# Optimization experiments

Hardware: AMD Instinct MI355X
Metric: run time of the kernel (lower is better)

## Reference

```python
import jax, jax.numpy as jnp
import numpy as np

B, H, W, C = 4, 64, 64, 128  # input feature map; num_heads == filters == C


def setup_inputs() -> dict:
    key = jax.random.key(0)
    ks = jax.random.split(key, 5)
    x = jax.random.normal(ks[0], (B, H, W, C), dtype=jnp.float32)
    scale = 0.02  # keep QK^T logits in a sane range for softmax
    Wf = jax.random.normal(ks[1], (C, C), dtype=jnp.float32) * scale
    Wg = jax.random.normal(ks[2], (C, C), dtype=jnp.float32) * scale
    Wh = jax.random.normal(ks[3], (C, C), dtype=jnp.float32) * scale
    Wv = jax.random.normal(ks[4], (C, C), dtype=jnp.float32) * scale
    zeros = jnp.zeros((C,), dtype=jnp.float32)
    return {
        "x": x,
        "Wf": Wf, "bf": zeros,
        "Wg": Wg, "bg": zeros,
        "Wh": Wh, "bh": zeros,
        "Wv": Wv, "bv": zeros,
        "gamma": jnp.float32(0.01),
    }


def reference(x, Wf, bf, Wg, bg, Wh, bh, Wv, bv, gamma):
    b, h, w, c = x.shape
    n = h * w
    xf = x.reshape(b, n, c)  # 1x1 conv == per-pixel linear
    f = xf @ Wf + bf  # [b, n, heads]
    g = xf @ Wg + bg
    v = xf @ Wh + bh
    # full spatial self-attention, unscaled logits (as in the original)
    s = jnp.einsum("bnc,bmc->bnm", f, g)  # [b, n, n]
    att = jax.nn.softmax(s, axis=-1)
    ctx = jnp.einsum("bnm,bmc->bnc", att, v)  # [b, n, heads]
    ctx = gamma * ctx
    # 1x1 conv v (linear activation) + residual
    o = ctx @ Wv + bv + xf
    return o.reshape(b, h, w, -1)
```

## Files before the change

### kernel.cpp

```cpp
#include <hip/hip_runtime.h>
#include <hip/hip_bf16.h>


typedef __hip_bfloat16 bf16;
typedef unsigned char u8;
typedef unsigned int  u32;
typedef unsigned long long u64;
typedef float  floatx4 __attribute__((ext_vector_type(4)));
typedef short  shortx8 __attribute__((ext_vector_type(8)));
typedef short  shortx4 __attribute__((ext_vector_type(4)));
typedef u32    uintx4  __attribute__((ext_vector_type(4)));

#define CDIM 128
#define NROW 16384
#define NPB  4096
#define LDW  136
#define LDK  72
#define LDG8 144
#define LDV8 80
#define QTILE 128
#define NKT  64
#define OSCALE 0.125f

__device__ __forceinline__ short f2bf(float v) {
    union { __hip_bfloat16 h; short s; } u; u.h = __float2bfloat16(v); return u.s;
}
__device__ __forceinline__ float bf2f(short s) {
    union { short s2; __hip_bfloat16 h; } u; u.s2 = s; return __bfloat162float(u.h);
}
__device__ __forceinline__ u8 f2fp8(float v) {
    int p = __builtin_amdgcn_cvt_pk_fp8_f32(v, v, 0, false);
    return (u8)(p & 0xff);
}
__device__ __forceinline__ u32 f2fp8x4(float a, float b, float c, float d) {
    int w = __builtin_amdgcn_cvt_pk_fp8_f32(a, b, 0, false);
    w = __builtin_amdgcn_cvt_pk_fp8_f32(c, d, w, true);
    return (u32)w;
}

__global__ __launch_bounds__(256) void proj3_kernel(
    const float* __restrict__ x,
    const float* __restrict__ Wf, const float* __restrict__ bf_,
    const float* __restrict__ Wg, const float* __restrict__ bg_,
    const float* __restrict__ Wh, const float* __restrict__ bh_,
    u8* __restrict__ f8, u8* __restrict__ g8, u8* __restrict__ vT8)
{
    __shared__ bf16 wt[128 * LDW];

    const int t    = threadIdx.x;
    const int wave = t >> 6, lane = t & 63;
    const int quad = lane >> 4, l16 = lane & 15;
    const int mtx    = blockIdx.x >> 8;
    const int rowblk = (blockIdx.x & 255) * 64;
    const int row    = rowblk + wave * 16 + l16;

    const float* Ws[3] = {Wf, Wg, Wh};
    const float* Bs[3] = {bf_, bg_, bh_};
    const float* W    = Ws[mtx];
    const float* bias = Bs[mtx];

    for (int i = t; i < 128 * 32; i += 256) {
        int k = i >> 5, n0 = (i & 31) * 4;
        floatx4 wv = *(const floatx4*)(W + k * CDIM + n0);
#pragma unroll
        for (int j = 0; j < 4; ++j)
            *(short*)&wt[(n0 + j) * LDW + k] = f2bf(wv[j]);
    }

    shortx8 afr[4];
    {
        const float* xp = x + (size_t)row * CDIM + quad * 8;
#pragma unroll
        for (int kc = 0; kc < 4; ++kc) {
            floatx4 u = *(const floatx4*)(xp + kc * 32);
            floatx4 w = *(const floatx4*)(xp + kc * 32 + 4);
            shortx8 a;
            a[0]=f2bf(u[0]); a[1]=f2bf(u[1]); a[2]=f2bf(u[2]); a[3]=f2bf(u[3]);
            a[4]=f2bf(w[0]); a[5]=f2bf(w[1]); a[6]=f2bf(w[2]); a[7]=f2bf(w[3]);
            afr[kc] = a;
        }
    }
    __syncthreads();

    floatx4 acc[8];
#pragma unroll
    for (int nt = 0; nt < 8; ++nt) acc[nt] = (floatx4){0.f, 0.f, 0.f, 0.f};
#pragma unroll
    for (int nt = 0; nt < 8; ++nt) {
        const bf16* wrow = &wt[(nt * 16 + l16) * LDW + quad * 8];
#pragma unroll
        for (int kc = 0; kc < 4; ++kc) {
            shortx8 b = *(const shortx8*)(wrow + kc * 32);
            acc[nt] = __builtin_amdgcn_mfma_f32_16x16x32_bf16(afr[kc], b, acc[nt], 0, 0, 0);
        }
    }

    if (mtx < 2) {
        u8* dst = (mtx == 0) ? f8 : g8;
#pragma unroll
        for (int nt = 0; nt < 8; ++nt) {
            int col = nt * 16 + l16;
            float bv_ = bias[col];
#pragma unroll
            for (int r = 0; r < 4; ++r) {
                int orow = rowblk + wave * 16 + quad * 4 + r;
                dst[(size_t)orow * CDIM + col] = f2fp8(acc[nt][r] + bv_);
            }
        }
    } else {
        __syncthreads();
        u8* vt8 = (u8*)wt;
        const int nloc0 = wave * 16 + quad * 4;
#pragma unroll
        for (int nt = 0; nt < 8; ++nt) {
            int ch = nt * 16 + l16;
            float bv_ = bias[ch];
            *(u32*)&vt8[ch * LDV8 + nloc0] =
                f2fp8x4(acc[nt][0] + bv_, acc[nt][1] + bv_,
                        acc[nt][2] + bv_, acc[nt][3] + bv_);
        }
        __syncthreads();
        const int ch  = t >> 1;
        const int off = (t & 1) * 32;
        const int batch = rowblk >> 12;
        const int n0 = (rowblk & 4095) + off;
        u8* dst = &vT8[((size_t)batch * CDIM + ch) * NPB + n0];
        const u8* src = &vt8[ch * LDV8 + off];
#pragma unroll
        for (int j = 0; j < 2; ++j)
            *(uintx4*)(dst + j * 16) = *(const uintx4*)(src + j * 16);
    }
}

__global__ __launch_bounds__(256, 3) void attn_kernel(
    const u8* __restrict__ f8, const u8* __restrict__ g8,
    const u8* __restrict__ vT8,
    u8* __restrict__ Opart8, float* __restrict__ lbuf, int nsplit)
{
    __shared__ u8 gs8[64 * LDG8];
    __shared__ u8 vs8[128 * LDV8];
    __shared__ u8 ps8[4 * 32 * LDV8];

    const int t    = threadIdx.x;
    const int wave = t >> 6, lane = t & 63;
    const int quad = lane >> 4, l16 = lane & 15;
    const int qg    = blockIdx.x;
    const int split = blockIdx.y;
    const int b  = qg >> 5;
    const int qt = qg & 31;
    const int qbase = b * NPB + qt * QTILE + wave * 32;

    const int kt0 = (split * NKT) / nsplit;
    const int kt1 = ((split + 1) * NKT) / nsplit;

    u64 qf[2][4];
#pragma unroll
    for (int sub = 0; sub < 2; ++sub) {
        const u8* qp = f8 + (size_t)(qbase + sub * 16 + l16) * CDIM + quad * 8;
#pragma unroll
        for (int kc = 0; kc < 4; ++kc) qf[sub][kc] = *(const u64*)(qp + kc * 32);
    }

    floatx4 o[2][8];
#pragma unroll
    for (int sub = 0; sub < 2; ++sub)
#pragma unroll
        for (int ct = 0; ct < 8; ++ct) o[sub][ct] = (floatx4){0.f, 0.f, 0.f, 0.f};
    float lacc[2] = {0.f, 0.f};

    const u8* gptr = g8 + (size_t)b * NPB * CDIM;
    const u8* vptr = vT8 + (size_t)b * CDIM * NPB;

    const int gk = t >> 2, go = (t & 3) * 32;
    const int vch = t >> 1, vo = (t & 1) * 32;

    shortx8 gx[2], vx[2];
#pragma unroll
    for (int i = 0; i < 2; ++i) {
        gx[i] = *(const shortx8*)&gptr[(size_t)(kt0 * 64 + gk) * CDIM + go + i * 16];
        vx[i] = *(const shortx8*)&vptr[(size_t)vch * NPB + kt0 * 64 + vo + i * 16];
    }

    for (int kt = kt0; kt < kt1; ++kt) {
        __syncthreads();
#pragma unroll
        for (int i = 0; i < 2; ++i) {
            *(shortx8*)&gs8[gk * LDG8 + go + i * 16] = gx[i];
            *(shortx8*)&vs8[vch * LDV8 + vo + i * 16] = vx[i];
        }
        if (kt + 1 < kt1) {
            const int ktn = kt + 1;
#pragma unroll
            for (int i = 0; i < 2; ++i) {
                gx[i] = *(const shortx8*)&gptr[(size_t)(ktn * 64 + gk) * CDIM + go + i * 16];
                vx[i] = *(const shortx8*)&vptr[(size_t)vch * NPB + ktn * 64 + vo + i * 16];
            }
        }
        __syncthreads();

        floatx4 s[2][4];
#pragma unroll
        for (int sub = 0; sub < 2; ++sub)
#pragma unroll
            for (int nt = 0; nt < 4; ++nt) s[sub][nt] = (floatx4){0.f, 0.f, 0.f, 0.f};
#pragma unroll
        for (int nt = 0; nt < 4; ++nt) {
            const u8* grow = &gs8[(nt * 16 + l16) * LDG8 + quad * 8];
#pragma unroll
            for (int kc = 0; kc < 4; ++kc) {
                u64 gfr = *(const u64*)(grow + kc * 32);
                s[0][nt] = __builtin_amdgcn_mfma_f32_16x16x32_fp8_fp8(
                    (long)gfr, (long)qf[0][kc], s[0][nt], 0, 0, 0);
                s[1][nt] = __builtin_amdgcn_mfma_f32_16x16x32_fp8_fp8(
                    (long)gfr, (long)qf[1][kc], s[1][nt], 0, 0, 0);
            }
        }

#pragma unroll
        for (int sub = 0; sub < 2; ++sub) {
            u8* pw = &ps8[(wave * 32 + sub * 16 + l16) * LDV8 + quad * 4];
#pragma unroll
            for (int nt = 0; nt < 4; ++nt) {
                float p0 = __expf(s[sub][nt][0]);
                float p1 = __expf(s[sub][nt][1]);
                float p2 = __expf(s[sub][nt][2]);
                float p3 = __expf(s[sub][nt][3]);
                lacc[sub] += (p0 + p1) + (p2 + p3);
                *(u32*)&pw[nt * 16] = f2fp8x4(p0, p1, p2, p3);
            }
        }

        u64 pa[2][2];
#pragma unroll
        for (int sub = 0; sub < 2; ++sub) {
            const u8* pr = &ps8[(wave * 32 + sub * 16 + l16) * LDV8 + quad * 8];
            pa[sub][0] = *(const u64*)pr;
            pa[sub][1] = *(const u64*)(pr + 32);
        }

#pragma unroll
        for (int ct = 0; ct < 8; ++ct) {
            const u8* vrow = &vs8[(ct * 16 + l16) * LDV8 + quad * 8];
#pragma unroll
            for (int kc2 = 0; kc2 < 2; ++kc2) {
                u64 vfr = *(const u64*)(vrow + kc2 * 32);
                o[0][ct] = __builtin_amdgcn_mfma_f32_16x16x32_fp8_fp8(
                    (long)pa[0][kc2], (long)vfr, o[0][ct], 0, 0, 0);
                o[1][ct] = __builtin_amdgcn_mfma_f32_16x16x32_fp8_fp8(
                    (long)pa[1][kc2], (long)vfr, o[1][ct], 0, 0, 0);
            }
        }
    }

    const size_t pbase = ((size_t)qg * nsplit + split) * QTILE * CDIM;
#pragma unroll
    for (int sub = 0; sub < 2; ++sub)
#pragma unroll
        for (int ct = 0; ct < 8; ++ct) {
            int col = ct * 16 + l16;
#pragma unroll
            for (int r = 0; r < 4; ++r) {
                int rl = wave * 32 + sub * 16 + quad * 4 + r;
                Opart8[pbase + (size_t)rl * CDIM + col] = f2fp8(o[sub][ct][r] * OSCALE);
            }
        }
    float* lb = lbuf + ((size_t)qg * nsplit + split) * QTILE;
#pragma unroll
    for (int sub = 0; sub < 2; ++sub) {
        float v = lacc[sub];
        v += __shfl_xor(v, 16);
        v += __shfl_xor(v, 32);
        if (quad == 0) lb[wave * 32 + sub * 16 + l16] = v;
    }
}

__global__ __launch_bounds__(256) void out_kernel(
    const u8* __restrict__ Opart8, const float* __restrict__ lbuf,
    const float* __restrict__ Wv, const float* __restrict__ bv,
    const float* __restrict__ x, const float* __restrict__ gamma,
    float* __restrict__ out, int nsplit)
{
    __shared__ bf16 wt[128 * LDW];

    const int t    = threadIdx.x;
    const int wave = t >> 6, lane = t & 63;
    const int quad = lane >> 4, l16 = lane & 15;
    const int rowblk = blockIdx.x * 64;
    const int row    = rowblk + wave * 16 + l16;

    const float gm = gamma[0];
    for (int i = t; i < 128 * 32; i += 256) {
        int k = i >> 5, n0 = (i & 31) * 4;
        floatx4 wv4 = *(const floatx4*)(Wv + k * CDIM + n0);
#pragma unroll
        for (int j = 0; j < 4; ++j)
            *(short*)&wt[(n0 + j) * LDW + k] = f2bf(wv4[j] * gm);
    }

    const int qg = row >> 7, rl = row & 127;
    float L = 0.f;
    for (int s = 0; s < nsplit; ++s)
        L += lbuf[((size_t)qg * nsplit + s) * QTILE + rl];
    const float inv = 8.0f / L;

    shortx8 afr[4];
#pragma unroll
    for (int kc = 0; kc < 4; ++kc) {
        float a8[8] = {0,0,0,0,0,0,0,0};
        for (int s = 0; s < nsplit; ++s) {
            const u8* p = &Opart8[(((size_t)qg * nsplit + s) * QTILE + rl) * CDIM + quad * 8 + kc * 32];
            u32 lo = *(const u32*)p;
            u32 hi = *(const u32*)(p + 4);
            a8[0] += __builtin_amdgcn_cvt_f32_fp8(lo, 0);
            a8[1] += __builtin_amdgcn_cvt_f32_fp8(lo, 1);
            a8[2] += __builtin_amdgcn_cvt_f32_fp8(lo, 2);
            a8[3] += __builtin_amdgcn_cvt_f32_fp8(lo, 3);
            a8[4] += __builtin_amdgcn_cvt_f32_fp8(hi, 0);
            a8[5] += __builtin_amdgcn_cvt_f32_fp8(hi, 1);
            a8[6] += __builtin_amdgcn_cvt_f32_fp8(hi, 2);
            a8[7] += __builtin_amdgcn_cvt_f32_fp8(hi, 3);
        }
        shortx8 a;
#pragma unroll
        for (int j = 0; j < 8; ++j) a[j] = f2bf(a8[j] * inv);
        afr[kc] = a;
    }
    __syncthreads();

    floatx4 acc[8];
#pragma unroll
    for (int nt = 0; nt < 8; ++nt) acc[nt] = (floatx4){0.f, 0.f, 0.f, 0.f};
#pragma unroll
    for (int nt = 0; nt < 8; ++nt) {
        const bf16* wrow = &wt[(nt * 16 + l16) * LDW + quad * 8];
#pragma unroll
        for (int kc = 0; kc < 4; ++kc) {
            shortx8 b = *(const shortx8*)(wrow + kc * 32);
            acc[nt] = __builtin_amdgcn_mfma_f32_16x16x32_bf16(afr[kc], b, acc[nt], 0, 0, 0);
        }
    }

#pragma unroll
    for (int nt = 0; nt < 8; ++nt) {
        int col = nt * 16 + l16;
        float bias = bv[col];
#pragma unroll
        for (int r = 0; r < 4; ++r) {
            int orow = rowblk + wave * 16 + quad * 4 + r;
            size_t idx = (size_t)orow * CDIM + col;
            out[idx] = acc[nt][r] + bias + x[idx];
        }
    }
}

extern "C" void kernel_launch(void* const* d_in, const int* in_sizes, int n_in,
                              void* d_out, int out_size, void* d_ws, size_t ws_size,
                              hipStream_t stream)
{
    const float* x   = (const float*)d_in[0];
    const float* Wf  = (const float*)d_in[1];
    const float* bf_ = (const float*)d_in[2];
    const float* Wg  = (const float*)d_in[3];
    const float* bg_ = (const float*)d_in[4];
    const float* Wh  = (const float*)d_in[5];
    const float* bh_ = (const float*)d_in[6];
    const float* Wv  = (const float*)d_in[7];
    const float* bv  = (const float*)d_in[8];
    const float* gm  = (const float*)d_in[9];
    float* out = (float*)d_out;

    const size_t need6 = (size_t)3 * NROW * CDIM
                       + (size_t)128 * 6 * QTILE * CDIM
                       + (size_t)128 * 6 * QTILE * 4;
    const int nsplit = (ws_size >= need6) ? 6 : 4;

    u8*   f8    = (u8*)d_ws;
    u8*   g8    = f8 + (size_t)NROW * CDIM;
    u8*   vT8   = g8 + (size_t)NROW * CDIM;
    u8*   Opart8 = vT8 + (size_t)NROW * CDIM;
    float* lbuf = (float*)(Opart8 + (size_t)128 * nsplit * QTILE * CDIM);

    proj3_kernel<<<768, 256, 0, stream>>>(x, Wf, bf_, Wg, bg_, Wh, bh_, f8, g8, vT8);
    attn_kernel<<<dim3(128, nsplit), 256, 0, stream>>>(f8, g8, vT8, Opart8, lbuf, nsplit);
    out_kernel<<<256, 256, 0, stream>>>(Opart8, lbuf, Wv, bv, x, gm, out, nsplit);
}
```

Before: 141.6 us.

## Use gfx950 scaled f8f6f4 MFMA (16x16x128, 32x32x64) in attention kernel

Replaces the 16x16x32 fp8 MFMAs in the QK and PV products of the attention kernel with the MI355X scaled f8f6f4 MFMA instructions at unit scale: 16x16x128 for QK and 32x32x64 for PV. Operand fragments are now loaded as 32-byte vectors, and the output accumulator and epilogue are re-laid out for the 32x32 tile. This cuts the number of MFMA issues and LDS fragment loads per key tile. In exchange it relies on the unit-scale encoding and the new operand and output lane layouts being correct.

```diff
diff --git a/kernel.cpp b/kernel.cpp
--- a/kernel.cpp
+++ b/kernel.cpp
@@ -6,21 +6,30 @@
 typedef unsigned char u8;
 typedef unsigned int  u32;
 typedef unsigned long long u64;
-typedef float  floatx4 __attribute__((ext_vector_type(4)));
+typedef float  floatx4  __attribute__((ext_vector_type(4)));
+typedef float  floatx16 __attribute__((ext_vector_type(16)));
 typedef short  shortx8 __attribute__((ext_vector_type(8)));
 typedef short  shortx4 __attribute__((ext_vector_type(4)));
 typedef u32    uintx4  __attribute__((ext_vector_type(4)));
+typedef int    intx8   __attribute__((ext_vector_type(8)));
 
 #define CDIM 128
 #define NROW 16384
 #define NPB  4096
 #define LDW  136
-#define LDK  72
 #define LDG8 144
 #define LDV8 80
 #define QTILE 128
 #define NKT  64
 #define OSCALE 0.125f
+#define UNIT_SCALE 0x7F7F7F7F
+
+#define MFMA_QK(a, b, c) \
+    __builtin_amdgcn_mfma_scale_f32_16x16x128_f8f6f4((a), (b), (c), 0, 0, \
+        0, UNIT_SCALE, 0, UNIT_SCALE)
+#define MFMA_PV(a, b, c) \
+    __builtin_amdgcn_mfma_scale_f32_32x32x64_f8f6f4((a), (b), (c), 0, 0, \
+        0, UNIT_SCALE, 0, UNIT_SCALE)
 
 __device__ __forceinline__ short f2bf(float v) {
     union { __hip_bfloat16 h; short s; } u; u.h = __float2bfloat16(v); return u.s;
@@ -36,6 +45,14 @@
     int w = __builtin_amdgcn_cvt_pk_fp8_f32(a, b, 0, false);
     w = __builtin_amdgcn_cvt_pk_fp8_f32(c, d, w, true);
     return (u32)w;
+}
+__device__ __forceinline__ intx8 ld32(const u8* p) {
+    uintx4 a = *(const uintx4*)p;
+    uintx4 b = *(const uintx4*)(p + 16);
+    intx8 r;
+    r[0] = (int)a[0]; r[1] = (int)a[1]; r[2] = (int)a[2]; r[3] = (int)a[3];
+    r[4] = (int)b[0]; r[5] = (int)b[1]; r[6] = (int)b[2]; r[7] = (int)b[3];
+    return r;
 }
 
 __global__ __launch_bounds__(256) void proj3_kernel(
@@ -144,6 +161,7 @@
     const int t    = threadIdx.x;
     const int wave = t >> 6, lane = t & 63;
     const int quad = lane >> 4, l16 = lane & 15;
+    const int c31  = lane & 31, hf = lane >> 5;
     const int qg    = blockIdx.x;
     const int split = blockIdx.y;
     const int b  = qg >> 5;
@@ -153,19 +171,16 @@
     const int kt0 = (split * NKT) / nsplit;
     const int kt1 = ((split + 1) * NKT) / nsplit;
 
-    u64 qf[2][4];
-#pragma unroll
-    for (int sub = 0; sub < 2; ++sub) {
-        const u8* qp = f8 + (size_t)(qbase + sub * 16 + l16) * CDIM + quad * 8;
-#pragma unroll
-        for (int kc = 0; kc < 4; ++kc) qf[sub][kc] = *(const u64*)(qp + kc * 32);
-    }
-
-    floatx4 o[2][8];
+    intx8 qf8[2];
 #pragma unroll
     for (int sub = 0; sub < 2; ++sub)
-#pragma unroll
-        for (int ct = 0; ct < 8; ++ct) o[sub][ct] = (floatx4){0.f, 0.f, 0.f, 0.f};
+        qf8[sub] = ld32(f8 + (size_t)(qbase + sub * 16 + l16) * CDIM + quad * 32);
+
+    floatx16 o[4];
+#pragma unroll
+    for (int ct = 0; ct < 4; ++ct)
+#pragma unroll
+        for (int i = 0; i < 16; ++i) o[ct][i] = 0.f;
     float lacc[2] = {0.f, 0.f};
 
     const u8* gptr = g8 + (size_t)b * NPB * CDIM;
@@ -200,20 +215,15 @@
 
         floatx4 s[2][4];
 #pragma unroll
-        for (int sub = 0; sub < 2; ++sub)
-#pragma unroll
-            for (int nt = 0; nt < 4; ++nt) s[sub][nt] = (floatx4){0.f, 0.f, 0.f, 0.f};
-#pragma unroll
         for (int nt = 0; nt < 4; ++nt) {
-            const u8* grow = &gs8[(nt * 16 + l16) * LDG8 + quad * 8];
-#pragma unroll
-            for (int kc = 0; kc < 4; ++kc) {
-                u64 gfr = *(const u64*)(grow + kc * 32);
-                s[0][nt] = __builtin_amdgcn_mfma_f32_16x16x32_fp8_fp8(
-                    (long)gfr, (long)qf[0][kc], s[0][nt], 0, 0, 0);
-                s[1][nt] = __builtin_amdgcn_mfma_f32_16x16x32_fp8_fp8(
-                    (long)gfr, (long)qf[1][kc], s[1][nt], 0, 0, 0);
-            }
+            s[0][nt] = (floatx4){0.f, 0.f, 0.f, 0.f};
+            s[1][nt] = (floatx4){0.f, 0.f, 0.f, 0.f};
+        }
+#pragma unroll
+        for (int nt = 0; nt < 4; ++nt) {
+            intx8 gf = ld32(&gs8[(nt * 16 + l16) * LDG8 + quad * 32]);
+            s[0][nt] = MFMA_QK(gf, qf8[0], s[0][nt]);
+            s[1][nt] = MFMA_QK(gf, qf8[1], s[1][nt]);
         }
 
 #pragma unroll
@@ -230,40 +240,25 @@
             }
         }
 
-        u64 pa[2][2];
-#pragma unroll
-        for (int sub = 0; sub < 2; ++sub) {
-            const u8* pr = &ps8[(wave * 32 + sub * 16 + l16) * LDV8 + quad * 8];
-            pa[sub][0] = *(const u64*)pr;
-            pa[sub][1] = *(const u64*)(pr + 32);
-        }
-
-#pragma unroll
-        for (int ct = 0; ct < 8; ++ct) {
-            const u8* vrow = &vs8[(ct * 16 + l16) * LDV8 + quad * 8];
-#pragma unroll
-            for (int kc2 = 0; kc2 < 2; ++kc2) {
-                u64 vfr = *(const u64*)(vrow + kc2 * 32);
-                o[0][ct] = __builtin_amdgcn_mfma_f32_16x16x32_fp8_fp8(
-                    (long)pa[0][kc2], (long)vfr, o[0][ct], 0, 0, 0);
-                o[1][ct] = __builtin_amdgcn_mfma_f32_16x16x32_fp8_fp8(
-                    (long)pa[1][kc2], (long)vfr, o[1][ct], 0, 0, 0);
-            }
+        intx8 pa8 = ld32(&ps8[(wave * 32 + c31) * LDV8 + hf * 32]);
+
+#pragma unroll
+        for (int ct = 0; ct < 4; ++ct) {
+            intx8 vf = ld32(&vs8[(ct * 32 + c31) * LDV8 + hf * 32]);
+            o[ct] = MFMA_PV(pa8, vf, o[ct]);
         }
     }
 
     const size_t pbase = ((size_t)qg * nsplit + split) * QTILE * CDIM;
 #pragma unroll
-    for (int sub = 0; sub < 2; ++sub)
-#pragma unroll
-        for (int ct = 0; ct < 8; ++ct) {
-            int col = ct * 16 + l16;
-#pragma unroll
-            for (int r = 0; r < 4; ++r) {
-                int rl = wave * 32 + sub * 16 + quad * 4 + r;
-                Opart8[pbase + (size_t)rl * CDIM + col] = f2fp8(o[sub][ct][r] * OSCALE);
-            }
-        }
+    for (int ct = 0; ct < 4; ++ct) {
+        int col = ct * 32 + c31;
+#pragma unroll
+        for (int i = 0; i < 16; ++i) {
+            int rl = wave * 32 + (i & 3) + 8 * (i >> 2) + 4 * hf;
+            Opart8[pbase + (size_t)rl * CDIM + col] = f2fp8(o[ct][i] * OSCALE);
+        }
+    }
     float* lb = lbuf + ((size_t)qg * nsplit + split) * QTILE;
 #pragma unroll
     for (int sub = 0; sub < 2; ++sub) {
```

Result: faster. 132.0 us (-6.8%).
